# Performance work log

Measured on AMD Instinct MI355X. Metric: run time of the kernel, lower is better.

## Reference

```python
import jax, jax.numpy as jnp
import numpy as np


def setup_inputs() -> dict:
    key = jax.random.key(0)
    k1, k2, k3 = jax.random.split(key, 3)
    x = jax.random.normal(k1, (8192, 2048), dtype=jnp.float32)
    w = jax.random.normal(k2, (4096, 2048), dtype=jnp.float32) * 0.02  # [out, in]
    b = jax.random.normal(k3, (4096,), dtype=jnp.float32) * 0.01
    return {"x": x, "w": w, "b": b}


def reference(x, w, b):
    # Straight-through binarization: forward uses sign(w), gradient flows as identity.
    binary_w = w + jax.lax.stop_gradient(jnp.sign(w) - w)  # [out, in], values in {-1, 0, 1}
    # F.linear: x @ W^T + b
    return jnp.einsum("ni,oi->no", x, binary_w) + b
```

## Files before the change

kernel.cpp:

```cpp
#include <hip/hip_runtime.h>
#include <hip/hip_bf16.h>
#include <stdint.h>

typedef __bf16 bf16x8 __attribute__((ext_vector_type(8)));
typedef float  f32x16 __attribute__((ext_vector_type(16)));


__device__ __forceinline__ uint32_t rn2_bf16(uint32_t lo, uint32_t hi) {
  uint32_t rlo = (lo + 0x7FFFu + ((lo >> 16) & 1u)) >> 16;
  uint32_t rhi = (hi + 0x7FFFu + ((hi >> 16) & 1u)) >> 16;
  return (rhi << 16) | (rlo & 0xFFFFu);
}

__device__ __forceinline__ uint32_t sign2_bf16(uint32_t lo, uint32_t hi) {
  uint32_t slo = (lo & 0x7FFFFFFFu) ? (0x3F80u | ((lo >> 16) & 0x8000u)) : 0u;
  uint32_t shi = (hi & 0x7FFFFFFFu) ? (0x3F80u | ((hi >> 16) & 0x8000u)) : 0u;
  return (shi << 16) | slo;
}

__device__ __forceinline__ void gl16(const void* g, void* l) {
  __builtin_amdgcn_global_load_lds(
      (const __attribute__((address_space(1))) uint32_t*)g,
      (__attribute__((address_space(3))) uint32_t*)l,
      16, 0, 0);
}


__global__ void prep_frag(const float* __restrict__ x, uint4* __restrict__ xf, int Mx,
                          const float* __restrict__ w, uint4* __restrict__ wf, int Nw,
                          int K) {
  const int kpw = K >> 6;
  const long nxc = ((long)Mx * K) >> 3;
  const long nwc = ((long)Nw * K) >> 3;
  const long stride = (long)gridDim.x * blockDim.x;
  for (long c = (long)blockIdx.x * blockDim.x + threadIdx.x; c < nxc + nwc; c += stride) {
    const bool isX = (c < nxc);
    const float* src = isX ? x : w;
    uint4* dst = isX ? xf : wf;
    const int rows32 = (isX ? Mx : Nw) >> 5;
    const long cc = isX ? c : (c - nxc);

    const int t = (int)(cc & 63);
    const long wv = cc >> 6;
    const int band = (int)(wv / kpw);
    const int kg = (int)(wv % kpw);
    const int row = band * 8 + (t & 7);
    const int k8 = kg * 8 + (t >> 3);

    const int kt = k8 >> 3, ks = (k8 >> 1) & 3, sub = k8 & 1;
    const int mb = row >> 5, r = row & 31;
    const long out16 = ((long)(kt * rows32 + mb) * 4 + ks) * 64 + sub * 32 + r;

    const uint4* s = reinterpret_cast<const uint4*>(src + (long)row * K + k8 * 8);
    uint4 a = s[0], b = s[1];
    uint4 o;
    if (isX) {
      o.x = rn2_bf16(a.x, a.y); o.y = rn2_bf16(a.z, a.w);
      o.z = rn2_bf16(b.x, b.y); o.w = rn2_bf16(b.z, b.w);
    } else {
      o.x = sign2_bf16(a.x, a.y); o.y = sign2_bf16(a.z, a.w);
      o.z = sign2_bf16(b.x, b.y); o.w = sign2_bf16(b.z, b.w);
    }
    dst[out16] = o;
  }
}


#define BARX()  asm volatile("s_barrier" ::: "memory")
#define VM0()   asm volatile("s_waitcnt vmcnt(0)" ::: "memory")
#define VMN8()  asm volatile("s_waitcnt vmcnt(8)" ::: "memory")

__global__ __launch_bounds__(512, 2) void gemm256(
    const uint16_t* __restrict__ Af,
    const uint16_t* __restrict__ Bf,
    const float* __restrict__ bias,
    float* __restrict__ C,
    int M, int N, int K) {
  __shared__ alignas(16) uint8_t L[131072];
  uint8_t* Lb = L;

  const int tid  = threadIdx.x;
  const int lane = tid & 63;
  const int w    = tid >> 6;
  const int wr   = w >> 2;
  const int wc   = w & 3;
  const int l31  = lane & 31;
  const int lhi  = lane >> 5;

  const int nbx = N >> 8;
  const int nwg = nbx * (M >> 8);
  const int bid = blockIdx.x;
  const int swb = (bid & 7) * (nwg >> 3) + (bid >> 3);
  const size_t m0 = (size_t)(swb / nbx) << 8;
  const size_t n0 = (size_t)(swb % nbx) << 8;

  const int NT = K >> 6;
  const size_t ktA = (size_t)(M >> 5) * 4096;
  const size_t ktB = (size_t)(N >> 5) * 4096;
  const char* Abase = (const char*)Af + (m0 >> 5) * 4096;
  const char* Bbase = (const char*)Bf + (n0 >> 5) * 4096;

  const int wB = w << 11;
  const int g0 = wB + lane * 16;
  const int g1 = g0 + 1024;

#define STG(LOFF, SRC) do { \
    gl16((SRC) + g0, Lb + (LOFF) + wB); \
    gl16((SRC) + g1, Lb + (LOFF) + wB + 1024); } while (0)

#define FRA32(d, i, q) (*reinterpret_cast<const bf16x8*>( \
    Lb + (d) * 65536 + wr * 16384 + (i) * 4096 + (q) * 1024 + lane * 16))
#define FRB32(d, j, q) (*reinterpret_cast<const bf16x8*>( \
    Lb + (d) * 65536 + 32768 + wc * 8192 + (j) * 4096 + (q) * 1024 + lane * 16))

#define RDA(DST, d, q) do { \
    _Pragma("unroll") \
    for (int i = 0; i < 4; ++i) DST[i] = FRA32(d, i, q); } while (0)
#define RDB(DST, d, q) do { \
    _Pragma("unroll") \
    for (int j = 0; j < 2; ++j) DST[j] = FRB32(d, j, q); } while (0)

  f32x16 acc[4][2] = {};

#define QM(A4, B2) do { \
    __builtin_amdgcn_s_setprio(1); \
    _Pragma("unroll") \
    for (int i = 0; i < 4; ++i) \
      _Pragma("unroll") \
      for (int j = 0; j < 2; ++j) \
        acc[i][j] = __builtin_amdgcn_mfma_f32_32x32x16_bf16( \
            A4[i], B2[j], acc[i][j], 0, 0, 0); \
    __builtin_amdgcn_s_setprio(0); } while (0)

  STG(0,      Abase);
  STG(16384,  Abase + 16384);
  STG(32768,  Bbase);
  STG(49152,  Bbase + 16384);
  STG(65536,  Abase + ktA);
  STG(81920,  Abase + ktA + 16384);
  STG(98304,  Bbase + ktB);
  STG(114688, Bbase + ktB + 16384);
  VMN8();
  BARX();

  bf16x8 S0a[4], S0b[2], S1a[4], S1b[2], S2a[4], S2b[2], S3a[4], S3b[2];
  RDA(S0a, 0, 0); RDB(S0b, 0, 0);
  RDA(S1a, 0, 1); RDB(S1b, 0, 1);

  const int T2 = K >> 7;
  for (int t = 0; t < T2; ++t) {
    const int u2 = 2 * t + 2, u3 = 2 * t + 3;
    const char* A2 = Abase + (size_t)(u2 < NT ? u2 : NT - 1) * ktA;
    const char* B2 = Bbase + (size_t)(u2 < NT ? u2 : NT - 1) * ktB;
    const char* A3 = Abase + (size_t)(u3 < NT ? u3 : NT - 1) * ktA;
    const char* B3 = Bbase + (size_t)(u3 < NT ? u3 : NT - 1) * ktB;

    QM(S0a, S0b);
    RDA(S2a, 0, 2); RDB(S2b, 0, 2);
    BARX();

    QM(S1a, S1b);
    RDA(S3a, 0, 3); RDB(S3b, 0, 3);
    VM0();
    BARX();

    QM(S2a, S2b);
    RDA(S0a, 1, 0); RDB(S0b, 1, 0);
    STG(0, A2);
    STG(16384, A2 + 16384);
    BARX();

    QM(S3a, S3b);
    RDA(S1a, 1, 1); RDB(S1b, 1, 1);
    STG(32768, B2);
    STG(49152, B2 + 16384);
    BARX();

    QM(S0a, S0b);
    RDA(S2a, 1, 2); RDB(S2b, 1, 2);
    BARX();

    QM(S1a, S1b);
    RDA(S3a, 1, 3); RDB(S3b, 1, 3);
    VM0();
    BARX();

    QM(S2a, S2b);
    RDA(S0a, 0, 0); RDB(S0b, 0, 0);
    STG(65536, A3);
    STG(81920, A3 + 16384);
    BARX();

    QM(S3a, S3b);
    RDA(S1a, 0, 1); RDB(S1b, 0, 1);
    STG(98304, B3);
    STG(114688, B3 + 16384);
    BARX();
  }
  VM0();

#pragma unroll
  for (int i = 0; i < 4; ++i) {
#pragma unroll
    for (int j2 = 0; j2 < 2; ++j2) {
      const size_t col = n0 + wc * 64 + j2 * 32 + l31;
      const float bv = bias[col];
      const size_t rbase = m0 + wr * 128 + i * 32 + lhi * 4;
#pragma unroll
      for (int r = 0; r < 16; ++r) {
        const size_t row = rbase + (r & 3) + 8 * (r >> 2);
        C[row * N + col] = acc[i][j2][r] + bv;
      }
    }
  }
}

__global__ void gemm_naive(const float* __restrict__ x, const float* __restrict__ w,
                           const float* __restrict__ b, float* __restrict__ out,
                           int M, int N, int K) {
  int n = blockIdx.x * blockDim.x + threadIdx.x;
  int m = blockIdx.y;
  if (n >= N || m >= M) return;
  float acc = 0.f;
  for (int k = 0; k < K; ++k) {
    float wv = w[(size_t)n * K + k];
    float s = (wv > 0.f) ? 1.f : ((wv < 0.f) ? -1.f : 0.f);
    acc += x[(size_t)m * K + k] * s;
  }
  out[(size_t)m * N + n] = acc + b[n];
}

extern "C" void kernel_launch(void* const* d_in, const int* in_sizes, int n_in,
                              void* d_out, int out_size, void* d_ws, size_t ws_size,
                              hipStream_t stream) {
  const float* x = (const float*)d_in[0];
  const float* w = (const float*)d_in[1];
  const float* b = (const float*)d_in[2];
  float* out = (float*)d_out;

  const int N = in_sizes[2];
  const int K = in_sizes[1] / N;
  const int M = in_sizes[0] / K;

  const size_t need = ((size_t)M * K + (size_t)N * K) * sizeof(uint16_t);
  const bool big_ok = (M % 256 == 0) && (N % 256 == 0) && (K % 256 == 0) &&
                      (((M / 256) * (N / 256)) % 8 == 0) && (ws_size >= need);
  if (!big_ok) {
    hipLaunchKernelGGL(gemm_naive, dim3((N + 255) / 256, M), dim3(256), 0, stream,
                       x, w, b, out, M, N, K);
    return;
  }

  uint16_t* Xf = (uint16_t*)d_ws;
  uint16_t* Wf = Xf + (size_t)M * K;

  hipLaunchKernelGGL(prep_frag, dim3(2048), dim3(256), 0, stream,
                     x, (uint4*)Xf, M, w, (uint4*)Wf, N, K);

  hipLaunchKernelGGL(gemm256, dim3((M / 256) * (N / 256)), dim3(512), 0, stream,
                     Xf, Wf, b, out, M, N, K);
}
```

Baseline: 145.9 us.

## Switch GEMM to 16x16x32 MFMA with new fragment layout and 8-phase pipeline

Replaces the 32x32x16 bf16 MFMA inner loop with 16x16x32 MFMAs, changing the pre-pack fragment layout so each 256-row band stores 16-row fragments contiguously per 32-wide k half. The main loop is restructured into eight phases that each issue one staging load, wait with explicit lgkmcnt/vmcnt counts, and are bracketed by barriers and sched_barriers. The aim is finer-grained overlap of global-to-LDS copies with MFMA work and a different register footprint. In exchange there are more barriers per k-tile, more LDS reads of B are interleaved, and correctness depends on the new prep and consumer layouts matching.

```diff
diff --git a/kernel.cpp b/kernel.cpp
--- a/kernel.cpp
+++ b/kernel.cpp
@@ -3,7 +3,7 @@
 #include <stdint.h>
 
 typedef __bf16 bf16x8 __attribute__((ext_vector_type(8)));
-typedef float  f32x16 __attribute__((ext_vector_type(16)));
+typedef float  f32x4  __attribute__((ext_vector_type(4)));
 
 
 __device__ __forceinline__ uint32_t rn2_bf16(uint32_t lo, uint32_t hi) {
@@ -37,19 +37,20 @@
     const bool isX = (c < nxc);
     const float* src = isX ? x : w;
     uint4* dst = isX ? xf : wf;
-    const int rows32 = (isX ? Mx : Nw) >> 5;
+    const int nbands = (isX ? Mx : Nw) >> 8;
     const long cc = isX ? c : (c - nxc);
 
     const int t = (int)(cc & 63);
     const long wv = cc >> 6;
-    const int band = (int)(wv / kpw);
+    const int band8 = (int)(wv / kpw);
     const int kg = (int)(wv % kpw);
-    const int row = band * 8 + (t & 7);
+    const int row = band8 * 8 + (t & 7);
     const int k8 = kg * 8 + (t >> 3);
 
-    const int kt = k8 >> 3, ks = (k8 >> 1) & 3, sub = k8 & 1;
-    const int mb = row >> 5, r = row & 31;
-    const long out16 = ((long)(kt * rows32 + mb) * 4 + ks) * 64 + sub * 32 + r;
+    const int kt = k8 >> 3, kk = (k8 >> 2) & 1, k8p = k8 & 3;
+    const int bb = row >> 8, mf16 = (row >> 4) & 15, r16 = row & 15;
+    const long out16 = ((long)(kt * nbands + bb)) * 2048 + kk * 1024 + mf16 * 64 +
+                       k8p * 16 + r16;
 
     const uint4* s = reinterpret_cast<const uint4*>(src + (long)row * K + k8 * 8);
     uint4 a = s[0], b = s[1];
@@ -66,9 +67,14 @@
 }
 
 
-#define BARX()  asm volatile("s_barrier" ::: "memory")
+#define BARX()  do { __builtin_amdgcn_s_barrier(); \
+                     __builtin_amdgcn_sched_barrier(0); } while (0)
+#define LGK0()  do { asm volatile("s_waitcnt lgkmcnt(0)" ::: "memory"); \
+                     __builtin_amdgcn_sched_barrier(0); } while (0)
 #define VM0()   asm volatile("s_waitcnt vmcnt(0)" ::: "memory")
-#define VMN8()  asm volatile("s_waitcnt vmcnt(8)" ::: "memory")
+#define VMN6()  asm volatile("s_waitcnt vmcnt(6)" ::: "memory")
+#define VMN10() asm volatile("s_waitcnt vmcnt(10)" ::: "memory")
+#define MF16(a, b, c) __builtin_amdgcn_mfma_f32_16x16x32_bf16((a), (b), (c), 0, 0, 0)
 
 __global__ __launch_bounds__(512, 2) void gemm256(
     const uint16_t* __restrict__ Af,
@@ -84,8 +90,8 @@
   const int w    = tid >> 6;
   const int wr   = w >> 2;
   const int wc   = w & 3;
-  const int l31  = lane & 31;
-  const int lhi  = lane >> 5;
+  const int l15  = lane & 15;
+  const int l4   = lane >> 4;
 
   const int nbx = N >> 8;
   const int nwg = nbx * (M >> 8);
@@ -95,10 +101,10 @@
   const size_t n0 = (size_t)(swb % nbx) << 8;
 
   const int NT = K >> 6;
-  const size_t ktA = (size_t)(M >> 5) * 4096;
-  const size_t ktB = (size_t)(N >> 5) * 4096;
-  const char* Abase = (const char*)Af + (m0 >> 5) * 4096;
-  const char* Bbase = (const char*)Bf + (n0 >> 5) * 4096;
+  const size_t ktA = (size_t)(M >> 8) * 32768;
+  const size_t ktB = (size_t)(N >> 8) * 32768;
+  const char* Abase = (const char*)Af + (m0 >> 8) * 32768;
+  const char* Bbase = (const char*)Bf + (n0 >> 8) * 32768;
 
   const int wB = w << 11;
   const int g0 = wB + lane * 16;
@@ -108,109 +114,74 @@
     gl16((SRC) + g0, Lb + (LOFF) + wB); \
     gl16((SRC) + g1, Lb + (LOFF) + wB + 1024); } while (0)
 
-#define FRA32(d, i, q) (*reinterpret_cast<const bf16x8*>( \
-    Lb + (d) * 65536 + wr * 16384 + (i) * 4096 + (q) * 1024 + lane * 16))
-#define FRB32(d, j, q) (*reinterpret_cast<const bf16x8*>( \
-    Lb + (d) * 65536 + 32768 + wc * 8192 + (j) * 4096 + (q) * 1024 + lane * 16))
-
-#define RDA(DST, d, q) do { \
+#define FRA(d, i, kk) (*reinterpret_cast<const bf16x8*>( \
+    Lb + (d) * 65536 + (kk) * 16384 + (wr * 8 + (i)) * 1024 + lane * 16))
+#define FRB(d, j, kk) (*reinterpret_cast<const bf16x8*>( \
+    Lb + (d) * 65536 + 32768 + (kk) * 16384 + (wc * 4 + (j)) * 1024 + lane * 16))
+
+  f32x4 acc[8][4] = {};
+  bf16x8 aR[4], bR[4];
+
+#define PHASE(d, kk, h, doB, STGL, STGS, doVMN) do { \
+    if (doB) { \
+      _Pragma("unroll") \
+      for (int j = 0; j < 4; ++j) bR[j] = FRB(d, j, kk); \
+    } \
     _Pragma("unroll") \
-    for (int i = 0; i < 4; ++i) DST[i] = FRA32(d, i, q); } while (0)
-#define RDB(DST, d, q) do { \
-    _Pragma("unroll") \
-    for (int j = 0; j < 2; ++j) DST[j] = FRB32(d, j, q); } while (0)
-
-  f32x16 acc[4][2] = {};
-
-#define QM(A4, B2) do { \
+    for (int i = 0; i < 4; ++i) aR[i] = FRA(d, (h) * 4 + i, kk); \
+    STG(STGL, STGS); \
+    if (doVMN) VMN10(); \
+    BARX(); \
+    LGK0(); \
     __builtin_amdgcn_s_setprio(1); \
     _Pragma("unroll") \
     for (int i = 0; i < 4; ++i) \
       _Pragma("unroll") \
-      for (int j = 0; j < 2; ++j) \
-        acc[i][j] = __builtin_amdgcn_mfma_f32_32x32x16_bf16( \
-            A4[i], B2[j], acc[i][j], 0, 0, 0); \
-    __builtin_amdgcn_s_setprio(0); } while (0)
+      for (int j = 0; j < 4; ++j) \
+        acc[(h) * 4 + i][j] = MF16(aR[i], bR[j], acc[(h) * 4 + i][j]); \
+    __builtin_amdgcn_s_setprio(0); \
+    BARX(); } while (0)
 
   STG(0,      Abase);
+  STG(32768,  Bbase);
   STG(16384,  Abase + 16384);
-  STG(32768,  Bbase);
   STG(49152,  Bbase + 16384);
   STG(65536,  Abase + ktA);
-  STG(81920,  Abase + ktA + 16384);
   STG(98304,  Bbase + ktB);
   STG(114688, Bbase + ktB + 16384);
-  VMN8();
+  VMN6();
   BARX();
-
-  bf16x8 S0a[4], S0b[2], S1a[4], S1b[2], S2a[4], S2b[2], S3a[4], S3b[2];
-  RDA(S0a, 0, 0); RDB(S0b, 0, 0);
-  RDA(S1a, 0, 1); RDB(S1b, 0, 1);
 
   const int T2 = K >> 7;
   for (int t = 0; t < T2; ++t) {
     const int u2 = 2 * t + 2, u3 = 2 * t + 3;
+    const char* A1 = Abase + (size_t)(2 * t + 1) * ktA;
     const char* A2 = Abase + (size_t)(u2 < NT ? u2 : NT - 1) * ktA;
     const char* B2 = Bbase + (size_t)(u2 < NT ? u2 : NT - 1) * ktB;
     const char* A3 = Abase + (size_t)(u3 < NT ? u3 : NT - 1) * ktA;
     const char* B3 = Bbase + (size_t)(u3 < NT ? u3 : NT - 1) * ktB;
 
-    QM(S0a, S0b);
-    RDA(S2a, 0, 2); RDB(S2b, 0, 2);
-    BARX();
-
-    QM(S1a, S1b);
-    RDA(S3a, 0, 3); RDB(S3b, 0, 3);
-    VM0();
-    BARX();
-
-    QM(S2a, S2b);
-    RDA(S0a, 1, 0); RDB(S0b, 1, 0);
-    STG(0, A2);
-    STG(16384, A2 + 16384);
-    BARX();
-
-    QM(S3a, S3b);
-    RDA(S1a, 1, 1); RDB(S1b, 1, 1);
-    STG(32768, B2);
-    STG(49152, B2 + 16384);
-    BARX();
-
-    QM(S0a, S0b);
-    RDA(S2a, 1, 2); RDB(S2b, 1, 2);
-    BARX();
-
-    QM(S1a, S1b);
-    RDA(S3a, 1, 3); RDB(S3b, 1, 3);
-    VM0();
-    BARX();
-
-    QM(S2a, S2b);
-    RDA(S0a, 0, 0); RDB(S0b, 0, 0);
-    STG(65536, A3);
-    STG(81920, A3 + 16384);
-    BARX();
-
-    QM(S3a, S3b);
-    RDA(S1a, 0, 1); RDB(S1b, 0, 1);
-    STG(98304, B3);
-    STG(114688, B3 + 16384);
-    BARX();
+    PHASE(0, 0, 0, 1, 81920,  A1 + 16384, 0);
+    PHASE(0, 0, 1, 0, 32768,  B2,         1);
+    PHASE(0, 1, 0, 1, 0,      A2,         0);
+    PHASE(0, 1, 1, 0, 49152,  B2 + 16384, 1);
+    PHASE(1, 0, 0, 1, 16384,  A2 + 16384, 0);
+    PHASE(1, 0, 1, 0, 98304,  B3,         1);
+    PHASE(1, 1, 0, 1, 65536,  A3,         0);
+    PHASE(1, 1, 1, 0, 114688, B3 + 16384, 1);
   }
   VM0();
 
 #pragma unroll
-  for (int i = 0; i < 4; ++i) {
+  for (int j = 0; j < 4; ++j) {
+    const size_t col = n0 + wc * 64 + j * 16 + l15;
+    const float bv = bias[col];
 #pragma unroll
-    for (int j2 = 0; j2 < 2; ++j2) {
-      const size_t col = n0 + wc * 64 + j2 * 32 + l31;
-      const float bv = bias[col];
-      const size_t rbase = m0 + wr * 128 + i * 32 + lhi * 4;
+    for (int mi = 0; mi < 8; ++mi) {
+      const size_t row0 = m0 + wr * 128 + mi * 16 + l4 * 4;
 #pragma unroll
-      for (int r = 0; r < 16; ++r) {
-        const size_t row = rbase + (r & 3) + 8 * (r >> 2);
-        C[row * N + col] = acc[i][j2][r] + bv;
-      }
+      for (int r = 0; r < 4; ++r)
+        C[(row0 + r) * N + col] = acc[mi][j][r] + bv;
     }
   }
 }
```

Result: slower. 151.0 us (+3.4%).
